# Kernel optimization log

Hardware: AMD Instinct MI355X
Metric: run time of the kernel (lower is better)

The kernel has to match this reference:

```python
import jax, jax.numpy as jnp
import numpy as np

N, E, G = 50000, 800000, 128
IN, HID, HEAD = 1280, 256, 4
DH = HID // HEAD
EPS = 1e-5
ATT_SCALE = 1.0 / np.sqrt(1280.0).astype(np.float32)  # hardcoded in source


def _seg_softmax(x, seg, n):
    # softmax over segments along axis 0; x: [K] or [K, H]
    m = jax.ops.segment_max(x, seg, num_segments=n)
    e = jnp.exp(x - m[seg])
    s = jax.ops.segment_sum(e, seg, num_segments=n)
    return e / s[seg]


def _bn(x, g, b):
    # eval-mode BatchNorm1d with init running stats (mean=0, var=1)
    return g * x * (1.0 / np.sqrt(1.0 + EPS)) + b


def _ln(x, g, b):
    mu = x.mean(-1, keepdims=True)
    var = ((x - mu) ** 2).mean(-1, keepdims=True)
    return g * (x - mu) / jnp.sqrt(var + EPS) + b


def setup_inputs() -> dict:
    key = jax.random.key(0)
    ks = jax.random.split(key, 40)
    rn = lambda i, shp, s=0.05: jax.random.normal(ks[i], shp, jnp.float32) * s
    inp = {
        "h": jax.random.normal(ks[0], (N, IN), jnp.float32),
        "gcn_w0": rn(1, (IN, HID)), "gcn_b0": rn(2, (HID,), 0.01),
        "gcn_w1": rn(3, (HID, HID)), "gcn_b1": rn(4, (HID,), 0.01),
        "bn_gcn0_g": 1.0 + rn(5, (HID,), 0.1), "bn_gcn0_b": rn(6, (HID,), 0.01),
        "bn_gcn1_g": 1.0 + rn(7, (HID,), 0.1), "bn_gcn1_b": rn(8, (HID,), 0.01),
        "gat_w0": rn(9, (IN, HID)), "gat_al0": rn(10, (HEAD, DH)), "gat_ar0": rn(11, (HEAD, DH)), "gat_bias0": rn(12, (HID,), 0.01),
        "gat_w1": rn(13, (HID, HID)), "gat_al1": rn(14, (HEAD, DH)), "gat_ar1": rn(15, (HEAD, DH)), "gat_bias1": rn(16, (HID,), 0.01),
        "bn_gat0_g": 1.0 + rn(17, (HID,), 0.1), "bn_gat0_b": rn(18, (HID,), 0.01),
        "bn_gat1_g": 1.0 + rn(19, (HID,), 0.1), "bn_gat1_b": rn(20, (HID,), 0.01),
        "gate_w": rn(21, (2 * HID, HID)), "gate_b": rn(22, (HID,), 0.01),
        "qw": rn(23, (HEAD, HID, HID)), "kw": rn(24, (HEAD, HID, HID)), "vw": rn(25, (HEAD, HID, HID)),
        "ct_w": rn(26, (HEAD * HID, HID)),
        "ff_w1": rn(27, (HID, 2 * HID)), "ff_b1": rn(28, (2 * HID,), 0.01),
        "ff_w2": rn(29, (2 * HID, HID)), "ff_b2": rn(30, (HID,), 0.01),
        "ln_g": 1.0 + rn(31, (HID,), 0.1), "ln_b": rn(32, (HID,), 0.01),
        "src": jax.random.randint(ks[33], (E,), 0, N, jnp.int32),
        "dst": jax.random.randint(ks[34], (E,), 0, N, jnp.int32),
        "gid": jnp.sort(jax.random.randint(ks[35], (N,), 0, G, jnp.int32)),
        "num_graphs": G,
    }
    return inp


def reference(h, gcn_w0, gcn_b0, gcn_w1, gcn_b1, bn_gcn0_g, bn_gcn0_b, bn_gcn1_g, bn_gcn1_b,
              gat_w0, gat_al0, gat_ar0, gat_bias0, gat_w1, gat_al1, gat_ar1, gat_bias1,
              bn_gat0_g, bn_gat0_b, bn_gat1_g, bn_gat1_b, gate_w, gate_b,
              qw, kw, vw, ct_w, ff_w1, ff_b1, ff_w2, ff_b2, ln_g, ln_b,
              src, dst, gid, num_graphs):
    n = h.shape[0]
    ones_e = jnp.ones(src.shape[0], h.dtype)
    # dgl.mean_nodes per graph
    cnt = jnp.clip(jax.ops.segment_sum(jnp.ones(n, h.dtype), gid, num_segments=num_graphs), 1.0)
    init_avg_h = jax.ops.segment_sum(h, gid, num_segments=num_graphs) / cnt[:, None]
    # GraphConv norm='both', degrees clamped to >=1
    deg_out = jnp.clip(jax.ops.segment_sum(ones_e, src, num_segments=n), 1.0)
    deg_in = jnp.clip(jax.ops.segment_sum(ones_e, dst, num_segments=n), 1.0)
    ns, nd = deg_out ** -0.5, deg_in ** -0.5

    def gcn(x, w, b):
        m = (x * ns[:, None]) @ w  # [N, HID]
        return jax.ops.segment_sum(m[src], dst, num_segments=n) * nd[:, None] + b

    hg = jax.nn.relu(_bn(gcn(h, gcn_w0, gcn_b0), bn_gcn0_g, bn_gcn0_b))
    hg = jax.nn.relu(_bn(gcn(hg, gcn_w1, gcn_b1), bn_gcn1_g, bn_gcn1_b)) + hg

    def gat(x, w, al, ar, b):
        f = (x @ w).reshape(n, HEAD, DH)
        el = (f * al).sum(-1)  # [N, HEAD]
        er = (f * ar).sum(-1)
        e = jax.nn.leaky_relu(el[src] + er[dst], 0.2)  # [E, HEAD]
        alpha = _seg_softmax(e, dst, n)  # edge softmax over incoming edges
        out = jax.ops.segment_sum(alpha[:, :, None] * f[src], dst, num_segments=n)
        return out.reshape(n, HID) + b

    ha = jax.nn.elu(_bn(gat(h, gat_w0, gat_al0, gat_ar0, gat_bias0), bn_gat0_g, bn_gat0_b))
    ha = jax.nn.elu(_bn(gat(ha, gat_w1, gat_al1, gat_ar1, gat_bias1), bn_gat1_g, bn_gat1_b)) + ha

    gate = jax.nn.sigmoid(jnp.concatenate([hg, ha], axis=1) @ gate_w + gate_b)
    x = gate * hg + (1.0 - gate) * ha  # residue_h

    # transformer_block: per-graph node softmax attention
    q = jnp.einsum('nd,hde->nhe', x, qw)
    k = jnp.einsum('nd,hde->nhe', x, kw)
    v = jnp.einsum('nd,hde->nhe', x, vw)
    att = (q * k).sum(-1) * ATT_SCALE  # [N, HEAD]
    alpha = _seg_softmax(att, gid, num_graphs)  # dgl.softmax_nodes per head
    mo = (v * alpha[:, :, None]).reshape(n, HEAD * HID) @ ct_w
    x1 = _ln(mo + x, ln_g, ln_b)
    x2 = _ln(jax.nn.relu(x1 @ ff_w1 + ff_b1) @ ff_w2 + ff_b2 + x1, ln_g, ln_b)

    readout = jax.ops.segment_sum(x2, gid, num_segments=num_graphs)
    return readout, init_avg_h
```

## Files before the change

### kernel.cpp

```cpp
#include <hip/hip_runtime.h>

#define NN 50000
#define NE 800000
#define NG 128
#define DIN 1280
#define HIDDEN 256
#define BNS 0.9999950000374997f
#define ATT_SCALE 0.027950849718747373f
#define LN_EPS 1e-5f

typedef __attribute__((ext_vector_type(8))) short short8;
typedef __attribute__((ext_vector_type(4))) float floatx4;

__device__ __forceinline__ float b2f(unsigned short u) {
  return __uint_as_float(((unsigned int)u) << 16);
}
__device__ __forceinline__ unsigned short f2b(float f) {
  unsigned int x = __float_as_uint(f);
  x += 0x7fffu + ((x >> 16) & 1u);
  return (unsigned short)(x >> 16);
}

__global__ void transpose_w_k(const float* __restrict__ src, unsigned short* __restrict__ dst,
                              int K, int Nc) {
  int idx = blockIdx.x * 256 + threadIdx.x;
  if (idx >= K * Nc) return;
  int n = idx / K, k = idx % K;
  dst[idx] = f2b(src[(size_t)k * Nc + n]);
}

__global__ void mw_k(const float* __restrict__ qw, const float* __restrict__ kw,
                     unsigned short* __restrict__ dst) {
  int col = blockIdx.x;
  int d = threadIdx.x;
  int hh = col >> 8, dp = col & 255;
  const float* qr = qw + ((size_t)hh * 256 + d) * 256;
  const float* kr = kw + ((size_t)hh * 256 + dp) * 256;
  float s = 0.f;
  for (int e = 0; e < 256; e += 4) {
    float4 a = *(const float4*)(qr + e);
    float4 b = *(const float4*)(kr + e);
    s += a.x * b.x + a.y * b.y + a.z * b.z + a.w * b.w;
  }
  dst[(size_t)col * 256 + d] = f2b(s);
}

__global__ void v_transpose_k(const float* __restrict__ vw, unsigned short* __restrict__ dst) {
  int idx = blockIdx.x * 256 + threadIdx.x;
  if (idx >= 1024 * 256) return;
  int r = idx >> 8;
  int d = idx & 255;
  int hh = r >> 8;
  int e2 = r & 255;
  dst[(size_t)(1024 + r) * 256 + d] = f2b(vw[((size_t)hh * 256 + d) * 256 + e2]);
}

__global__ void cvt_avg_k(const float* __restrict__ h, const int* __restrict__ gid,
                          unsigned short* __restrict__ h_bf, float* __restrict__ out1) {
  int row0 = blockIdx.x * 50;
  int tid = threadIdx.x;
  float acc[5] = {0, 0, 0, 0, 0};
  int cur_g = gid[row0];
  for (int r = 0; r < 50; ++r) {
    int row = row0 + r;
    int g = gid[row];
    if (g != cur_g) {
#pragma unroll
      for (int j = 0; j < 5; ++j) {
        atomicAdd(&out1[(size_t)cur_g * DIN + j * 256 + tid], acc[j]);
        acc[j] = 0.f;
      }
      cur_g = g;
    }
#pragma unroll
    for (int j = 0; j < 5; ++j) {
      float v = h[(size_t)row * DIN + j * 256 + tid];
      acc[j] += v;
      h_bf[(size_t)row * DIN + j * 256 + tid] = f2b(v);
    }
  }
#pragma unroll
  for (int j = 0; j < 5; ++j)
    atomicAdd(&out1[(size_t)cur_g * DIN + j * 256 + tid], acc[j]);
}

__global__ void div_avg_k(const int* __restrict__ start, float* __restrict__ out1) {
  int idx = blockIdx.x * 256 + threadIdx.x;
  if (idx >= NG * DIN) return;
  int g = idx / DIN;
// ... 57 lines not shown
                            int* __restrict__ row_ptr) {
  __shared__ int buf[256];
  int t = threadIdx.x;
  int v = (t < nb) ? bsum[t] : 0;
  buf[t] = v;
  __syncthreads();
  for (int off = 1; off < 256; off <<= 1) {
    int tv = (t >= off) ? buf[t - off] : 0;
    __syncthreads();
    buf[t] += tv;
    __syncthreads();
  }
  if (t < nb) boff[t] = buf[t] - v;
  if (t == 0) row_ptr[NN] = NE;
}

__global__ void scan_add_k(int* __restrict__ row_ptr, const int* __restrict__ boff) {
  int i = blockIdx.x * 256 + threadIdx.x;
  if (i >= NN) return;
  row_ptr[i] += boff[blockIdx.x];
}

__global__ void fill_csr_k(const int* __restrict__ src, const int* __restrict__ dst,
                           const int* __restrict__ row_ptr, int* __restrict__ fill,
                           int* __restrict__ csr_src, int e) {
  int i = blockIdx.x * 256 + threadIdx.x;
  if (i >= e) return;
  int d = dst[i];
  int pos = row_ptr[d] + atomicAdd(&fill[d], 1);
  csr_src[pos] = src[i];
}

template <int MODE>
__global__ __launch_bounds__(256, 2) void gemm_bf16(const unsigned short* __restrict__ A,
                                                    const unsigned short* __restrict__ Bt,
                                                    void* __restrict__ Cout,
                                                    const float* __restrict__ bias,
                                                    int M, int K, int Nc,
                                                    const unsigned short* __restrict__ xtile,
                                                    float* __restrict__ attp,
                                                    const float* __restrict__ ascale) {
  __shared__ unsigned short sbuf[16384];
  unsigned short* lA = sbuf;
  unsigned short* lB = sbuf + 8192;
  const int tid = threadIdx.x;
  const int n0 = blockIdx.x * 128;
  const int m0 = blockIdx.y * 128;
  const int w = tid >> 6;
  const int lane = tid & 63;
  const int wr = (w >> 1) * 64;
  const int wc = (w & 1) * 64;
  const int quad = lane >> 4;
  const int l15 = lane & 15;
  const int js = tid & 7;
  const int mbase = tid >> 3;

  floatx4 acc[4][4];
#pragma unroll
  for (int i = 0; i < 4; ++i)
#pragma unroll
    for (int j = 0; j < 4; ++j) acc[i][j] = (floatx4)0.0f;

  for (int k0 = 0; k0 < K; k0 += 64) {
    __syncthreads();
#pragma unroll
    for (int it = 0; it < 4; ++it) {
      int m = it * 32 + mbase;
      int gm = m0 + m;
      if (gm >= M) gm = M - 1;
      uint4 va = *(const uint4*)(A + (size_t)gm * K + k0 + js * 8);
      if (MODE == 5) {
        float s = ascale[(size_t)gm * 4 + (k0 >> 8)];
        unsigned short* pp = (unsigned short*)&va;
#pragma unroll
        for (int c = 0; c < 8; ++c) pp[c] = f2b(b2f(pp[c]) * s);
      }
      int ci_ = js * 128 + (m ^ js);
      *(uint4*)(lA + ci_ * 8) = va;
      int gn = n0 + m;
      uint4 vb = *(const uint4*)(Bt + (size_t)gn * K + k0 + js * 8);
      *(uint4*)(lB + ci_ * 8) = vb;
    }
    __syncthreads();
#pragma unroll
    for (int ks = 0; ks < 2; ++ks) {
      int kb = ks * 4 + quad;
      short8 af[4], bfr[4];
#pragma unroll
      for (int ri = 0; ri < 4; ++ri) {
        int r = wr + ri * 16 + l15;
        af[ri] = *(const short8*)(lA + (kb * 128 + (r ^ kb)) * 8);
      }
#pragma unroll
      for (int ci = 0; ci < 4; ++ci) {
        int c = wc + ci * 16 + l15;
        bfr[ci] = *(const short8*)(lB + (kb * 128 + (c ^ kb)) * 8);
      }
#pragma unroll
      for (int ri = 0; ri < 4; ++ri)
#pragma unroll
        for (int ci = 0; ci < 4; ++ci)
          acc[ri][ci] = __builtin_amdgcn_mfma_f32_16x16x32_bf16(af[ri], bfr[ci], acc[ri][ci], 0, 0, 0);
    }
  }

  if (MODE == 4 && n0 < 1024) {
    __syncthreads();
    int cb = n0 & 255;
#pragma unroll
    for (int it2 = 0; it2 < 8; ++it2) {
      int linear = it2 * 256 + tid;
      int rr = linear >> 4;
      int c8 = (linear & 15) * 8;
      int gr = m0 + rr;
      if (gr >= M) gr = M - 1;
      *(uint4*)(sbuf + rr * 128 + c8) = *(const uint4*)(xtile + (size_t)gr * 256 + cb + c8);
    }
    __syncthreads();
    int head = n0 >> 8;
#pragma unroll
    for (int ri = 0; ri < 4; ++ri) {
      int lrow = wr + ri * 16 + quad * 4;
#pragma unroll
      for (int r = 0; r < 4; ++r) {
        float p = 0.f;
#pragma unroll
        for (int ci = 0; ci < 4; ++ci)
          p += acc[ri][ci][r] * b2f(sbuf[(lrow + r) * 128 + wc + ci * 16 + l15]);
        p += __shfl_xor(p, 1);
        p += __shfl_xor(p, 2);
        p += __shfl_xor(p, 4);
        p += __shfl_xor(p, 8);
        if (l15 == 0) {
          int grow = m0 + lrow + r;
          if (grow < M) atomicAdd(&attp[(size_t)grow * 4 + head], p * ATT_SCALE);
        }
      }
    }
    return;
  }

#pragma unroll
  for (int ri = 0; ri < 4; ++ri) {
    int row = m0 + wr + ri * 16 + quad * 4;
#pragma unroll
    for (int ci = 0; ci < 4; ++ci) {
      int col = n0 + wc + ci * 16 + l15;
      float bv = (MODE == 2) ? bias[col] : 0.f;
#pragma unroll
      for (int r = 0; r < 4; ++r) {
        if (row + r < M) {
          float v = acc[ri][ci][r];
          if (MODE == 2) { v += bv; v = fmaxf(v, 0.f); }
          if (MODE == 1)
            ((float*)Cout)[(size_t)(row + r) * Nc + col] = v;
          else if (MODE == 4)
            ((unsigned short*)Cout)[(size_t)(row + r) * 1024 + col - 1024] = f2b(v);
          else
            ((unsigned short*)Cout)[(size_t)(row + r) * Nc + col] = f2b(v);
        }
      }
    }
  }
}

__global__ void gcn_agg_k(const unsigned short* __restrict__ m, int ldm,
                          const int* __restrict__ row_ptr, const int* __restrict__ csr_src,
                          const float* __restrict__ ns, const float* __restrict__ nd,
                          const float* __restrict__ bias,
                          const float* __restrict__ bng, const float* __restrict__ bnb,
                          const unsigned short* __restrict__ resid, int ldr,
                          unsigned short* __restrict__ out, int ldo) {
  int node = blockIdx.x * 4 + (threadIdx.x >> 6);
  if (node >= NN) return;
  int lane = threadIdx.x & 63;
  int s = row_ptr[node], e = row_ptr[node + 1];
  float a0 = 0, a1 = 0, a2 = 0, a3 = 0;
  for (int i = s; i < e; ++i) {
    int u = csr_src[i];
    float w = ns[u];
    ushort4 v = *(const ushort4*)(m + (size_t)u * ldm + lane * 4);
    a0 += w * b2f(v.x); a1 += w * b2f(v.y); a2 += w * b2f(v.z); a3 += w * b2f(v.w);
  }
  float ndv = nd[node];
  int col = lane * 4;
  float vals[4] = {a0, a1, a2, a3};
  ushort4 o;
#pragma unroll
  for (int c = 0; c < 4; ++c) {
    float v = vals[c] * ndv + bias[col + c];
    v = bng[col + c] * v * BNS + bnb[col + c];
    v = fmaxf(v, 0.f);
    if (resid) v += b2f(resid[(size_t)node * ldr + col + c]);
    ((unsigned short*)&o)[c] = f2b(v);
  }
  *(ushort4*)(out + (size_t)node * ldo + col) = o;
}

__global__ void elr_k(const unsigned short* __restrict__ f, int ldf,
                      const float* __restrict__ al, const float* __restrict__ ar,
                      float* __restrict__ elr) {
  int node = blockIdx.x * 4 + (threadIdx.x >> 6);
  if (node >= NN) return;
  int lane = threadIdx.x & 63;
  int head = lane >> 4;
  int col = lane * 4;
  int dcol = col & 63;
  ushort4 v = *(const ushort4*)(f + (size_t)node * ldf + col);
  float pl = 0, pr = 0;
#pragma unroll
  for (int c = 0; c < 4; ++c) {
    float x = b2f(((unsigned short*)&v)[c]);
    pl += x * al[head * 64 + dcol + c];
    pr += x * ar[head * 64 + dcol + c];
  }
#pragma unroll
  for (int off = 1; off < 16; off <<= 1) {
    pl += __shfl_xor(pl, off);
    pr += __shfl_xor(pr, off);
  }
  if ((lane & 15) == 0) {
    elr[(size_t)node * 8 + head] = pl;
    elr[(size_t)node * 8 + 4 + head] = pr;
  }
}

__global__ void gat_agg_k(const unsigned short* __restrict__ f, int ldf,
                          const int* __restrict__ row_ptr, const int* __restrict__ csr_src,
                          const float* __restrict__ elr,
                          const float* __restrict__ bias,
                          const float* __restrict__ bng, const float* __restrict__ bnb,
                          const unsigned short* __restrict__ resid, int ldr,
                          unsigned short* __restrict__ out, int ldo) {
  int node = blockIdx.x * 4 + (threadIdx.x >> 6);
  if (node >= NN) return;
  int lane = threadIdx.x & 63;
  int s = row_ptr[node], e = row_ptr[node + 1];
  float4 er = *(const float4*)(elr + (size_t)node * 8 + 4);
  float m0 = -1e30f, m1 = -1e30f, m2 = -1e30f, m3 = -1e30f;
  for (int i = s + lane; i < e; i += 64) {
    int u = csr_src[i];
    float4 el = *(const float4*)(elr + (size_t)u * 8);
    float t;
    t = el.x + er.x; t = t > 0.f ? t : 0.2f * t; m0 = fmaxf(m0, t);
    t = el.y + er.y; t = t > 0.f ? t : 0.2f * t; m1 = fmaxf(m1, t);
    t = el.z + er.z; t = t > 0.f ? t : 0.2f * t; m2 = fmaxf(m2, t);
    t = el.w + er.w; t = t > 0.f ? t : 0.2f * t; m3 = fmaxf(m3, t);
  }
#pragma unroll
  for (int off = 1; off < 64; off <<= 1) {
    m0 = fmaxf(m0, __shfl_xor(m0, off));
    m1 = fmaxf(m1, __shfl_xor(m1, off));
    m2 = fmaxf(m2, __shfl_xor(m2, off));
    m3 = fmaxf(m3, __shfl_xor(m3, off));
  }
  float s0 = 0, s1 = 0, s2 = 0, s3 = 0;
  for (int i = s + lane; i < e; i += 64) {
    int u = csr_src[i];
    float4 el = *(const float4*)(elr + (size_t)u * 8);
    float t;
    t = el.x + er.x; t = t > 0.f ? t : 0.2f * t; s0 += expf(t - m0);
    t = el.y + er.y; t = t > 0.f ? t : 0.2f * t; s1 += expf(t - m1);
    t = el.z + er.z; t = t > 0.f ? t : 0.2f * t; s2 += expf(t - m2);
    t = el.w + er.w; t = t > 0.f ? t : 0.2f * t; s3 += expf(t - m3);
  }
#pragma unroll
  for (int off = 1; off < 64; off <<= 1) {
    s0 += __shfl_xor(s0, off);
    s1 += __shfl_xor(s1, off);
    s2 += __shfl_xor(s2, off);
    s3 += __shfl_xor(s3, off);
  }
  int head = lane >> 4;
  float erh = head == 0 ? er.x : head == 1 ? er.y : head == 2 ? er.z : er.w;
  float mh = head == 0 ? m0 : head == 1 ? m1 : head == 2 ? m2 : m3;
  float sh = head == 0 ? s0 : head == 1 ? s1 : head == 2 ? s2 : s3;
  float inv_sh = (sh > 0.f) ? 1.f / sh : 0.f;
  float a0 = 0, a1 = 0, a2 = 0, a3 = 0;
  for (int i = s; i < e; ++i) {
    int u = csr_src[i];
    float t = elr[(size_t)u * 8 + head] + erh;
    t = t > 0.f ? t : 0.2f * t;
    float wgt = expf(t - mh) * inv_sh;
    ushort4 v = *(const ushort4*)(f + (size_t)u * ldf + lane * 4);
    a0 += wgt * b2f(v.x); a1 += wgt * b2f(v.y); a2 += wgt * b2f(v.z); a3 += wgt * b2f(v.w);
  }
  int col = lane * 4;
  float vals[4] = {a0, a1, a2, a3};
  ushort4 o;
#pragma unroll
  for (int c = 0; c < 4; ++c) {
    float v = vals[c] + bias[col + c];
    v = bng[col + c] * v * BNS + bnb[col + c];
    v = (v > 0.f) ? v : (expf(v) - 1.f);
    if (resid) v += b2f(resid[(size_t)node * ldr + col + c]);
    ((unsigned short*)&o)[c] = f2b(v);
  }
  *(ushort4*)(out + (size_t)node * ldo + col) = o;
}

__global__ void combine_k(const unsigned short* __restrict__ glogit, const float* __restrict__ gate_b,
                          const unsigned short* __restrict__ xcat,
                          unsigned short* __restrict__ xb) {
  int idx = blockIdx.x * 256 + threadIdx.x;
  if (idx >= NN * 64) return;
  int node = idx >> 6;
  int c = (idx & 63) * 4;
  ushort4 gl = *(const ushort4*)(glogit + (size_t)node * HIDDEN + c);
  ushort4 hgv = *(const ushort4*)(xcat + (size_t)node * 512 + c);
  ushort4 hav = *(const ushort4*)(xcat + (size_t)node * 512 + 256 + c);
  ushort4 ob;
  float g;
  g = 1.f / (1.f + expf(-(b2f(gl.x) + gate_b[c + 0]))); ob.x = f2b(g * b2f(hgv.x) + (1.f - g) * b2f(hav.x));
  g = 1.f / (1.f + expf(-(b2f(gl.y) + gate_b[c + 1]))); ob.y = f2b(g * b2f(hgv.y) + (1.f - g) * b2f(hav.y));
  g = 1.f / (1.f + expf(-(b2f(gl.z) + gate_b[c + 2]))); ob.z = f2b(g * b2f(hgv.z) + (1.f - g) * b2f(hav.z));
  g = 1.f / (1.f + expf(-(b2f(gl.w) + gate_b[c + 3]))); ob.w = f2b(g * b2f(hgv.w) + (1.f - g) * b2f(hav.w));
  *(ushort4*)(xb + (size_t)node * HIDDEN + c) = ob;
}

__global__ void gsoftmax_k(const float* __restrict__ att, const int* __restrict__ start,
                           float* __restrict__ alpha) {
  int g = blockIdx.x;
  int s = start[g], e = start[g + 1];
  int tid = threadIdx.x;
  __shared__ float red[256];
  __shared__ float mh[4], sh[4];
  float lm[4] = {-1e30f, -1e30f, -1e30f, -1e30f};
  for (int i = s + tid; i < e; i += 256) {
    float4 a = *(const float4*)(att + (size_t)i * 4);
    lm[0] = fmaxf(lm[0], a.x); lm[1] = fmaxf(lm[1], a.y);
    lm[2] = fmaxf(lm[2], a.z); lm[3] = fmaxf(lm[3], a.w);
  }
#pragma unroll
  for (int h = 0; h < 4; ++h) {
    red[tid] = lm[h]; __syncthreads();
    for (int off = 128; off > 0; off >>= 1) {
      if (tid < off) red[tid] = fmaxf(red[tid], red[tid + off]);
      __syncthreads();
    }
    if (tid == 0) mh[h] = red[0];
    __syncthreads();
  }
  float ls[4] = {0, 0, 0, 0};
  for (int i = s + tid; i < e; i += 256) {
    float4 a = *(const float4*)(att + (size_t)i * 4);
    ls[0] += expf(a.x - mh[0]); ls[1] += expf(a.y - mh[1]);
    ls[2] += expf(a.z - mh[2]); ls[3] += expf(a.w - mh[3]);
  }
#pragma unroll
  for (int h = 0; h < 4; ++h) {
// ... 52 lines not shown
  if (node >= NN) return;
  int lane = threadIdx.x & 63;
  int c = lane * 4;
  ushort4 a = *(const ushort4*)(ff2o + (size_t)node * HIDDEN + c);
  ushort4 xx = *(const ushort4*)(x1 + (size_t)node * HIDDEN + c);
  float v0 = b2f(a.x) + ffb2[c + 0] + b2f(xx.x), v1 = b2f(a.y) + ffb2[c + 1] + b2f(xx.y);
  float v2 = b2f(a.z) + ffb2[c + 2] + b2f(xx.z), v3 = b2f(a.w) + ffb2[c + 3] + b2f(xx.w);
  float sm = v0 + v1 + v2 + v3;
#pragma unroll
  for (int off = 1; off < 64; off <<= 1) sm += __shfl_xor(sm, off);
  float mu = sm * (1.f / 256.f);
  float d0 = v0 - mu, d1 = v1 - mu, d2 = v2 - mu, d3 = v3 - mu;
  float sq = d0 * d0 + d1 * d1 + d2 * d2 + d3 * d3;
#pragma unroll
  for (int off = 1; off < 64; off <<= 1) sq += __shfl_xor(sq, off);
  float inv = rsqrtf(sq * (1.f / 256.f) + LN_EPS);
  ushort4 ob;
  ob.x = f2b(g[c + 0] * d0 * inv + b[c + 0]);
  ob.y = f2b(g[c + 1] * d1 * inv + b[c + 1]);
  ob.z = f2b(g[c + 2] * d2 * inv + b[c + 2]);
  ob.w = f2b(g[c + 3] * d3 * inv + b[c + 3]);
  *(ushort4*)(x2 + (size_t)node * HIDDEN + c) = ob;
}

__global__ void readout_k(const unsigned short* __restrict__ x2, const int* __restrict__ start,
                          float* __restrict__ out0) {
  int g = blockIdx.x;
  int c = threadIdx.x;
  float acc = 0.f;
  for (int i = start[g]; i < start[g + 1]; ++i) acc += b2f(x2[(size_t)i * HIDDEN + c]);
  out0[(size_t)g * HIDDEN + c] = acc;
}

static const size_t OFF_BUFA   = 0;
static const size_t OFF_C01    = 128000000;
static const size_t OFF_HG0    = 179200000;
static const size_t OFF_HA0    = 204800000;
static const size_t OFF_M1     = 230400000;
static const size_t OFF_F1     = 256000000;
static const size_t OFF_XCAT   = 281600000;
static const size_t OFF_GLOGIT = 332800000;
static const size_t OFF_XB     = 358400000;
static const size_t OFF_MO     = 384000000;
static const size_t OFF_X1     = 409600000;
static const size_t OFF_ATT    = 435200000;
static const size_t OFF_ALPHA  = OFF_ATT + 800000;
static const size_t OFF_ELR0   = OFF_ALPHA + 800000;
static const size_t OFF_ELR1   = OFF_ELR0 + 1600000;
static const size_t OFF_START  = OFF_ELR1 + 1600000;
static const size_t OFF_DEGO   = OFF_START + 1024;
static const size_t OFF_DEGI   = OFF_DEGO + 200704;
static const size_t OFF_NS     = OFF_DEGI + 200704;
static const size_t OFF_ND     = OFF_NS + 200704;
static const size_t OFF_ROWP   = OFF_ND + 200704;
static const size_t OFF_FILL   = OFF_ROWP + 200704;
static const size_t OFF_BSUM   = OFF_FILL + 200704;
static const size_t OFF_BOFF   = OFF_BSUM + 1024;
static const size_t OFF_CSRS   = OFF_BOFF + 1024;
static const size_t OFF_W01T   = OFF_CSRS + 3200000;
static const size_t OFF_W1T    = OFF_W01T + 1310720;
static const size_t OFF_W1GT   = OFF_W1T + 131072;
static const size_t OFF_GATEWT = OFF_W1GT + 131072;
static const size_t OFF_WMVT   = OFF_GATEWT + 262144;
static const size_t OFF_CTWT   = OFF_WMVT + 1048576;
static const size_t OFF_FFW1T  = OFF_CTWT + 524288;
static const size_t OFF_FFW2T  = OFF_FFW1T + 262144;
static const size_t WS_NEED    = OFF_FFW2T + 262144;

extern "C" void kernel_launch(void* const* d_in, const int* in_sizes, int n_in,
                              void* d_out, int out_size, void* d_ws, size_t ws_size,
                              hipStream_t stream) {
  if (ws_size < WS_NEED) return;

  const float* h       = (const float*)d_in[0];
  const float* gcn_w0  = (const float*)d_in[1];
  const float* gcn_b0  = (const float*)d_in[2];
  const float* gcn_w1  = (const float*)d_in[3];
  const float* gcn_b1  = (const float*)d_in[4];
  const float* bn_gcn0_g = (const float*)d_in[5];
  const float* bn_gcn0_b = (const float*)d_in[6];
  const float* bn_gcn1_g = (const float*)d_in[7];
  const float* bn_gcn1_b = (const float*)d_in[8];
  const float* gat_w0  = (const float*)d_in[9];
  const float* gat_al0 = (const float*)d_in[10];
  const float* gat_ar0 = (const float*)d_in[11];
  const float* gat_bias0 = (const float*)d_in[12];
  const float* gat_w1  = (const float*)d_in[13];
  const float* gat_al1 = (const float*)d_in[14];
  const float* gat_ar1 = (const float*)d_in[15];
  const float* gat_bias1 = (const float*)d_in[16];
  const float* bn_gat0_g = (const float*)d_in[17];
  const float* bn_gat0_b = (const float*)d_in[18];
  const float* bn_gat1_g = (const float*)d_in[19];
  const float* bn_gat1_b = (const float*)d_in[20];
  const float* gate_w  = (const float*)d_in[21];
  const float* gate_b  = (const float*)d_in[22];
  const float* qw      = (const float*)d_in[23];
  const float* kw      = (const float*)d_in[24];
  const float* vw      = (const float*)d_in[25];
  const float* ct_w    = (const float*)d_in[26];
  const float* ff_w1   = (const float*)d_in[27];
  const float* ff_b1   = (const float*)d_in[28];
  const float* ff_w2   = (const float*)d_in[29];
  const float* ff_b2   = (const float*)d_in[30];
  const float* ln_g    = (const float*)d_in[31];
  const float* ln_b    = (const float*)d_in[32];
  const int* srcv = (const int*)d_in[33];
  const int* dstv = (const int*)d_in[34];
  const int* gid  = (const int*)d_in[35];

  char* ws = (char*)d_ws;
  unsigned short* h_bf = (unsigned short*)(ws + OFF_BUFA);
  unsigned short* yv   = (unsigned short*)(ws + OFF_BUFA);
  unsigned short* ff1o = (unsigned short*)(ws + OFF_BUFA);
  unsigned short* ff2o = (unsigned short*)(ws + OFF_BUFA + 51200000);
  unsigned short* x2   = (unsigned short*)(ws + OFF_BUFA + 76800000);
  unsigned short* c01  = (unsigned short*)(ws + OFF_C01);
  unsigned short* hg0  = (unsigned short*)(ws + OFF_HG0);
  unsigned short* ha0  = (unsigned short*)(ws + OFF_HA0);
  unsigned short* m1   = (unsigned short*)(ws + OFF_M1);
  unsigned short* f1   = (unsigned short*)(ws + OFF_F1);
  unsigned short* xcat = (unsigned short*)(ws + OFF_XCAT);
  unsigned short* glogit = (unsigned short*)(ws + OFF_GLOGIT);
  unsigned short* xb   = (unsigned short*)(ws + OFF_XB);
  unsigned short* mo   = (unsigned short*)(ws + OFF_MO);
  unsigned short* x1   = (unsigned short*)(ws + OFF_X1);
  float* att           = (float*)(ws + OFF_ATT);
  float* alpha         = (float*)(ws + OFF_ALPHA);
  float* elr0          = (float*)(ws + OFF_ELR0);
  float* elr1          = (float*)(ws + OFF_ELR1);
  int* start   = (int*)(ws + OFF_START);
  int* deg_out = (int*)(ws + OFF_DEGO);
  int* deg_in  = (int*)(ws + OFF_DEGI);
  float* ns    = (float*)(ws + OFF_NS);
  float* nd    = (float*)(ws + OFF_ND);
  int* row_ptr = (int*)(ws + OFF_ROWP);
  int* fill    = (int*)(ws + OFF_FILL);
  int* bsum    = (int*)(ws + OFF_BSUM);
  int* boff    = (int*)(ws + OFF_BOFF);
  int* csr_src = (int*)(ws + OFF_CSRS);
  unsigned short* w01t   = (unsigned short*)(ws + OFF_W01T);
  unsigned short* w1t    = (unsigned short*)(ws + OFF_W1T);
  unsigned short* w1gt   = (unsigned short*)(ws + OFF_W1GT);
  unsigned short* gatewt = (unsigned short*)(ws + OFF_GATEWT);
  unsigned short* wmvt   = (unsigned short*)(ws + OFF_WMVT);
  unsigned short* ctwt   = (unsigned short*)(ws + OFF_CTWT);
  unsigned short* ffw1t  = (unsigned short*)(ws + OFF_FFW1T);
  unsigned short* ffw2t  = (unsigned short*)(ws + OFF_FFW2T);

  float* out0 = (float*)d_out;
  float* out1 = out0 + NG * HIDDEN;

  hipMemsetAsync(deg_out, 0, NN * 4, stream);
  hipMemsetAsync(deg_in, 0, NN * 4, stream);
  hipMemsetAsync(fill, 0, NN * 4, stream);
  hipMemsetAsync(out1, 0, NG * DIN * 4, stream);
  hipMemsetAsync(att, 0, NN * 4 * 4, stream);

  transpose_w_k<<<(1280 * 256 + 255) / 256, 256, 0, stream>>>(gcn_w0, w01t, 1280, 256);
  transpose_w_k<<<(1280 * 256 + 255) / 256, 256, 0, stream>>>(gat_w0, w01t + 256 * 1280, 1280, 256);
  transpose_w_k<<<(256 * 256 + 255) / 256, 256, 0, stream>>>(gcn_w1, w1t, 256, 256);
  transpose_w_k<<<(256 * 256 + 255) / 256, 256, 0, stream>>>(gat_w1, w1gt, 256, 256);
  transpose_w_k<<<(512 * 256 + 255) / 256, 256, 0, stream>>>(gate_w, gatewt, 512, 256);
  mw_k<<<1024, 256, 0, stream>>>(qw, kw, wmvt);
  v_transpose_k<<<1024, 256, 0, stream>>>(vw, wmvt);
  transpose_w_k<<<(1024 * 256 + 255) / 256, 256, 0, stream>>>(ct_w, ctwt, 1024, 256);
  transpose_w_k<<<(256 * 512 + 255) / 256, 256, 0, stream>>>(ff_w1, ffw1t, 256, 512);
  transpose_w_k<<<(512 * 256 + 255) / 256, 256, 0, stream>>>(ff_w2, ffw2t, 512, 256);

  graph_bounds_k<<<(NN + 255) / 256, 256, 0, stream>>>(gid, start, NN);
  degrees_k<<<(NE + 255) / 256, 256, 0, stream>>>(srcv, dstv, deg_out, deg_in, NE);
  invsqrt_k<<<(NN + 255) / 256, 256, 0, stream>>>(deg_out, deg_in, ns, nd, NN);
  const int NB_SCAN = (NN + 255) / 256;
  scan_local_k<<<NB_SCAN, 256, 0, stream>>>(deg_in, row_ptr, bsum);
  scan_bsum_k<<<1, 256, 0, stream>>>(bsum, boff, NB_SCAN, row_ptr);
  scan_add_k<<<NB_SCAN, 256, 0, stream>>>(row_ptr, boff);
  fill_csr_k<<<(NE + 255) / 256, 256, 0, stream>>>(srcv, dstv, row_ptr, fill, csr_src, NE);

  cvt_avg_k<<<NN / 50, 256, 0, stream>>>(h, gid, h_bf, out1);
  div_avg_k<<<(NG * DIN + 255) / 256, 256, 0, stream>>>(start, out1);

  const int MB = (NN + 127) / 128;
  gemm_bf16<0><<<dim3(4, MB), 256, 0, stream>>>(h_bf, w01t, c01, nullptr, NN, 1280, 512,
                                                nullptr, nullptr, nullptr);
  gcn_agg_k<<<NN / 4, 256, 0, stream>>>(c01, 512, row_ptr, csr_src, ns, nd,
                                        gcn_b0, bn_gcn0_g, bn_gcn0_b, nullptr, 0, hg0, 256);
  elr_k<<<NN / 4, 256, 0, stream>>>(c01 + 256, 512, gat_al0, gat_ar0, elr0);
  gat_agg_k<<<NN / 4, 256, 0, stream>>>(c01 + 256, 512, row_ptr, csr_src, elr0,
                                        gat_bias0, bn_gat0_g, bn_gat0_b, nullptr, 0, ha0, 256);
  gemm_bf16<0><<<dim3(2, MB), 256, 0, stream>>>(hg0, w1t, m1, nullptr, NN, 256, 256,
                                                nullptr, nullptr, nullptr);
  gcn_agg_k<<<NN / 4, 256, 0, stream>>>(m1, 256, row_ptr, csr_src, ns, nd,
                                        gcn_b1, bn_gcn1_g, bn_gcn1_b, hg0, 256, xcat, 512);
  gemm_bf16<0><<<dim3(2, MB), 256, 0, stream>>>(ha0, w1gt, f1, nullptr, NN, 256, 256,
                                                nullptr, nullptr, nullptr);
  elr_k<<<NN / 4, 256, 0, stream>>>(f1, 256, gat_al1, gat_ar1, elr1);
  gat_agg_k<<<NN / 4, 256, 0, stream>>>(f1, 256, row_ptr, csr_src, elr1,
                                        gat_bias1, bn_gat1_g, bn_gat1_b, ha0, 256, xcat + 256, 512);
  gemm_bf16<0><<<dim3(2, MB), 256, 0, stream>>>(xcat, gatewt, glogit, nullptr, NN, 512, 256,
                                                nullptr, nullptr, nullptr);
  combine_k<<<NN / 4, 256, 0, stream>>>(glogit, gate_b, xcat, xb);
  gemm_bf16<4><<<dim3(16, MB), 256, 0, stream>>>(xb, wmvt, yv, nullptr, NN, 256, 2048,
                                                 xb, att, nullptr);
  gsoftmax_k<<<NG, 256, 0, stream>>>(att, start, alpha);
  gemm_bf16<5><<<dim3(2, MB), 256, 0, stream>>>(yv, ctwt, mo, nullptr, NN, 1024, 256,
                                                nullptr, nullptr, alpha);
  ln1_k<<<NN / 4, 256, 0, stream>>>(mo, xb, ln_g, ln_b, x1);
  gemm_bf16<2><<<dim3(4, MB), 256, 0, stream>>>(x1, ffw1t, ff1o, ff_b1, NN, 256, 512,
                                                nullptr, nullptr, nullptr);
  gemm_bf16<0><<<dim3(2, MB), 256, 0, stream>>>(ff1o, ffw2t, ff2o, nullptr, NN, 512, 256,
                                                nullptr, nullptr, nullptr);
  ln2_k<<<NN / 4, 256, 0, stream>>>(ff2o, ff_b2, x1, ln_g, ln_b, x2);
  readout_k<<<NG, 256, 0, stream>>>(x2, start, out0);
}
```

Measured before the change: 1.750 ms.

## Fuse elr and gate epilogues into GEMMs, batch layer-1 GEMMs, enlarge tiles

Several ideas land at once. GEMM tiles grow to 256x128 with one wave per 64 rows. The GAT el/er projections move into the GEMM epilogues (modes 6 and 7), which removes the elr kernels, and the gate sigmoid/combine moves into the gate GEMM epilogue. The two layer-1 GEMMs are merged into one launch over padded stacked buffers, and the weight transposes are batched into a single prep launch. The GAT edge softmax also drops its max-subtraction pass, which saves a full edge sweep but risks overflow in expf for large logits.

```diff
diff --git a/kernel.cpp b/kernel.cpp
--- a/kernel.cpp
+++ b/kernel.cpp
@@ -1,6 +1,7 @@
 #include <hip/hip_runtime.h>
 
 #define NN 50000
+#define NN2 50176
 #define NE 800000
 #define NG 128
 #define DIN 1280
@@ -21,12 +22,21 @@
   return (unsigned short)(x >> 16);
 }
 
-__global__ void transpose_w_k(const float* __restrict__ src, unsigned short* __restrict__ dst,
-                              int K, int Nc) {
+struct PrepJob { const float* s; unsigned short* d; int K; int Nc; int special; };
+struct PrepJobs { PrepJob j[9]; };
+
+__global__ void prep_k(PrepJobs P) {
+  PrepJob pj = P.j[blockIdx.y];
   int idx = blockIdx.x * 256 + threadIdx.x;
-  if (idx >= K * Nc) return;
-  int n = idx / K, k = idx % K;
-  dst[idx] = f2b(src[(size_t)k * Nc + n]);
+  if (idx >= pj.K * pj.Nc) return;
+  if (!pj.special) {
+    int n = idx / pj.K, k = idx % pj.K;
+    pj.d[idx] = f2b(pj.s[(size_t)k * pj.Nc + n]);
+  } else {
+    int r = idx >> 8, dd = idx & 255;
+    int hh = r >> 8, e2 = r & 255;
+    pj.d[idx] = f2b(pj.s[((size_t)hh * 256 + dd) * 256 + e2]);
+  }
 }
 
 __global__ void mw_k(const float* __restrict__ qw, const float* __restrict__ kw,
@@ -45,16 +55,6 @@
   dst[(size_t)col * 256 + d] = f2b(s);
 }
 
-__global__ void v_transpose_k(const float* __restrict__ vw, unsigned short* __restrict__ dst) {
-  int idx = blockIdx.x * 256 + threadIdx.x;
-  if (idx >= 1024 * 256) return;
-  int r = idx >> 8;
-  int d = idx & 255;
-  int hh = r >> 8;
-  int e2 = r & 255;
-  dst[(size_t)(1024 + r) * 256 + d] = f2b(vw[((size_t)hh * 256 + d) * 256 + e2]);
-}
-
 __global__ void cvt_avg_k(const float* __restrict__ h, const int* __restrict__ gid,
                           unsigned short* __restrict__ h_bf, float* __restrict__ out1) {
   int row0 = blockIdx.x * 50;
@@ -178,39 +178,46 @@
 }
 
 template <int MODE>
-__global__ __launch_bounds__(256, 2) void gemm_bf16(const unsigned short* __restrict__ A,
-                                                    const unsigned short* __restrict__ Bt,
-                                                    void* __restrict__ Cout,
-                                                    const float* __restrict__ bias,
-                                                    int M, int K, int Nc,
-                                                    const unsigned short* __restrict__ xtile,
-                                                    float* __restrict__ attp,
-                                                    const float* __restrict__ ascale) {
-  __shared__ unsigned short sbuf[16384];
+__global__ __launch_bounds__(256, 2) void gemm_bf16(
+    const unsigned short* __restrict__ A,
+    const unsigned short* __restrict__ Bt,
+    const unsigned short* __restrict__ Bt2,
+    void* __restrict__ Cout,
+    const float* __restrict__ bias,
+    int M, int K, int Nc,
+    const unsigned short* __restrict__ xaux,
+    float* __restrict__ faux,
+    const float* __restrict__ ascale,
+    const float* __restrict__ al, const float* __restrict__ ar,
+    int esplit) {
+  constexpr int SBN = (MODE == 4) ? 32768 : 24576;
+  __shared__ unsigned short sbuf[SBN];
   unsigned short* lA = sbuf;
-  unsigned short* lB = sbuf + 8192;
+  unsigned short* lB = sbuf + 16384;
   const int tid = threadIdx.x;
   const int n0 = blockIdx.x * 128;
-  const int m0 = blockIdx.y * 128;
+  const int m0 = blockIdx.y * 256;
   const int w = tid >> 6;
   const int lane = tid & 63;
-  const int wr = (w >> 1) * 64;
-  const int wc = (w & 1) * 64;
   const int quad = lane >> 4;
   const int l15 = lane & 15;
   const int js = tid & 7;
   const int mbase = tid >> 3;
-
-  floatx4 acc[4][4];
+  const int wrow = w * 64;
+
+  const unsigned short* Buse = Bt;
+  if (MODE == 7 && m0 >= esplit) Buse = Bt2;
+
+  floatx4 acc[4][8];
 #pragma unroll
   for (int i = 0; i < 4; ++i)
 #pragma unroll
-    for (int j = 0; j < 4; ++j) acc[i][j] = (floatx4)0.0f;
+    for (int j = 0; j < 8; ++j) acc[i][j] = (floatx4)0.0f;
 
   for (int k0 = 0; k0 < K; k0 += 64) {
     __syncthreads();
 #pragma unroll
-    for (int it = 0; it < 4; ++it) {
+    for (int it = 0; it < 8; ++it) {
       int m = it * 32 + mbase;
       int gm = m0 + m;
       if (gm >= M) gm = M - 1;
@@ -221,31 +228,33 @@
 #pragma unroll
         for (int c = 0; c < 8; ++c) pp[c] = f2b(b2f(pp[c]) * s);
       }
-      int ci_ = js * 128 + (m ^ js);
-      *(uint4*)(lA + ci_ * 8) = va;
-      int gn = n0 + m;
-      uint4 vb = *(const uint4*)(Bt + (size_t)gn * K + k0 + js * 8);
-      *(uint4*)(lB + ci_ * 8) = vb;
+      *(uint4*)(lA + (js * 256 + (m ^ js)) * 8) = va;
+    }
+#pragma unroll
+    for (int it = 0; it < 4; ++it) {
+      int n = it * 32 + mbase;
+      uint4 vb = *(const uint4*)(Buse + (size_t)(n0 + n) * K + k0 + js * 8);
+      *(uint4*)(lB + (js * 128 + (n ^ js)) * 8) = vb;
     }
     __syncthreads();
 #pragma unroll
     for (int ks = 0; ks < 2; ++ks) {
       int kb = ks * 4 + quad;
-      short8 af[4], bfr[4];
+      short8 af[4], bfr[8];
 #pragma unroll
       for (int ri = 0; ri < 4; ++ri) {
-        int r = wr + ri * 16 + l15;
-        af[ri] = *(const short8*)(lA + (kb * 128 + (r ^ kb)) * 8);
+        int r = wrow + ri * 16 + l15;
+        af[ri] = *(const short8*)(lA + (kb * 256 + (r ^ kb)) * 8);
       }
 #pragma unroll
-      for (int ci = 0; ci < 4; ++ci) {
-        int c = wc + ci * 16 + l15;
+      for (int ci = 0; ci < 8; ++ci) {
+        int c = ci * 16 + l15;
         bfr[ci] = *(const short8*)(lB + (kb * 128 + (c ^ kb)) * 8);
       }
 #pragma unroll
       for (int ri = 0; ri < 4; ++ri)
 #pragma unroll
-        for (int ci = 0; ci < 4; ++ci)
+        for (int ci = 0; ci < 8; ++ci)
           acc[ri][ci] = __builtin_amdgcn_mfma_f32_16x16x32_bf16(af[ri], bfr[ci], acc[ri][ci], 0, 0, 0);
     }
   }
@@ -254,32 +263,32 @@
     __syncthreads();
     int cb = n0 & 255;
 #pragma unroll
-    for (int it2 = 0; it2 < 8; ++it2) {
+    for (int it2 = 0; it2 < 16; ++it2) {
       int linear = it2 * 256 + tid;
       int rr = linear >> 4;
       int c8 = (linear & 15) * 8;
       int gr = m0 + rr;
       if (gr >= M) gr = M - 1;
-      *(uint4*)(sbuf + rr * 128 + c8) = *(const uint4*)(xtile + (size_t)gr * 256 + cb + c8);
+      *(uint4*)(sbuf + rr * 128 + c8) = *(const uint4*)(xaux + (size_t)gr * 256 + cb + c8);
     }
     __syncthreads();
     int head = n0 >> 8;
 #pragma unroll
     for (int ri = 0; ri < 4; ++ri) {
-      int lrow = wr + ri * 16 + quad * 4;
+      int lrow = wrow + ri * 16 + quad * 4;
 #pragma unroll
       for (int r = 0; r < 4; ++r) {
         float p = 0.f;
 #pragma unroll
-        for (int ci = 0; ci < 4; ++ci)
-          p += acc[ri][ci][r] * b2f(sbuf[(lrow + r) * 128 + wc + ci * 16 + l15]);
+        for (int ci = 0; ci < 8; ++ci)
+          p += acc[ri][ci][r] * b2f(sbuf[(lrow + r) * 128 + ci * 16 + l15]);
         p += __shfl_xor(p, 1);
         p += __shfl_xor(p, 2);
         p += __shfl_xor(p, 4);
         p += __shfl_xor(p, 8);
         if (l15 == 0) {
           int grow = m0 + lrow + r;
-          if (grow < M) atomicAdd(&attp[(size_t)grow * 4 + head], p * ATT_SCALE);
+          if (grow < M) atomicAdd(&faux[(size_t)grow * 4 + head], p * ATT_SCALE);
         }
       }
     }
@@ -288,22 +297,65 @@
 
 #pragma unroll
   for (int ri = 0; ri < 4; ++ri) {
-    int row = m0 + wr + ri * 16 + quad * 4;
-#pragma unroll
-    for (int ci = 0; ci < 4; ++ci) {
-      int col = n0 + wc + ci * 16 + l15;
-      float bv = (MODE == 2) ? bias[col] : 0.f;
+    int row = m0 + wrow + ri * 16 + quad * 4;
+#pragma unroll
+    for (int ci = 0; ci < 8; ++ci) {
+      int col = n0 + ci * 16 + l15;
+      float bv = (MODE == 2 || MODE == 3) ? bias[col] : 0.f;
 #pragma unroll
       for (int r = 0; r < 4; ++r) {
         if (row + r < M) {
           float v = acc[ri][ci][r];
-          if (MODE == 2) { v += bv; v = fmaxf(v, 0.f); }
-          if (MODE == 1)
-            ((float*)Cout)[(size_t)(row + r) * Nc + col] = v;
-          else if (MODE == 4)
+          if (MODE == 2) {
+            v += bv; v = fmaxf(v, 0.f);
+            ((unsigned short*)Cout)[(size_t)(row + r) * Nc + col] = f2b(v);
+          } else if (MODE == 3) {
+            float g = 1.f / (1.f + expf(-(v + bv)));
+            float hg = b2f(xaux[(size_t)(row + r) * 512 + col]);
+            float ha = b2f(xaux[(size_t)(row + r) * 512 + 256 + col]);
+            ((unsigned short*)Cout)[(size_t)(row + r) * 256 + col] = f2b(g * hg + (1.f - g) * ha);
+          } else if (MODE == 4) {
             ((unsigned short*)Cout)[(size_t)(row + r) * 1024 + col - 1024] = f2b(v);
-          else
+          } else {
             ((unsigned short*)Cout)[(size_t)(row + r) * Nc + col] = f2b(v);
+          }
+        }
+      }
+    }
+  }
+
+  if ((MODE == 6 && n0 >= esplit) || (MODE == 7 && m0 >= esplit)) {
+    int hbase = (MODE == 6) ? ((n0 - esplit) >> 6) : (n0 >> 6);
+#pragma unroll
+    for (int ri = 0; ri < 4; ++ri) {
+#pragma unroll
+      for (int r = 0; r < 4; ++r) {
+        int grow = m0 + wrow + ri * 16 + quad * 4 + r;
+        float pl0 = 0, pr0 = 0, pl1 = 0, pr1 = 0;
+#pragma unroll
+        for (int ci = 0; ci < 4; ++ci) {
+          float a0_ = acc[ri][ci][r];
+          float a1_ = acc[ri][ci + 4][r];
+          float w0l = al[hbase * 64 + ci * 16 + l15];
+          float w0r = ar[hbase * 64 + ci * 16 + l15];
+          float w1l = al[(hbase + 1) * 64 + ci * 16 + l15];
+          float w1r = ar[(hbase + 1) * 64 + ci * 16 + l15];
+          pl0 += a0_ * w0l; pr0 += a0_ * w0r;
+          pl1 += a1_ * w1l; pr1 += a1_ * w1r;
+        }
+#pragma unroll
+        for (int off = 1; off < 16; off <<= 1) {
+          pl0 += __shfl_xor(pl0, off); pr0 += __shfl_xor(pr0, off);
+          pl1 += __shfl_xor(pl1, off); pr1 += __shfl_xor(pr1, off);
+        }
+        if (l15 == 0) {
+          int erow = (MODE == 7) ? (grow - esplit) : grow;
+          if (erow >= 0 && erow < NN) {
+            faux[(size_t)erow * 8 + hbase] = pl0;
+            faux[(size_t)erow * 8 + 4 + hbase] = pr0;
+            faux[(size_t)erow * 8 + hbase + 1] = pl1;
+            faux[(size_t)erow * 8 + 5 + hbase] = pr1;
+          }
         }
       }
     }
@@ -343,34 +395,6 @@
   *(ushort4*)(out + (size_t)node * ldo + col) = o;
 }
 
-__global__ void elr_k(const unsigned short* __restrict__ f, int ldf,
-                      const float* __restrict__ al, const float* __restrict__ ar,
-                      float* __restrict__ elr) {
-  int node = blockIdx.x * 4 + (threadIdx.x >> 6);
-  if (node >= NN) return;
-  int lane = threadIdx.x & 63;
-  int head = lane >> 4;
-  int col = lane * 4;
-  int dcol = col & 63;
-  ushort4 v = *(const ushort4*)(f + (size_t)node * ldf + col);
-  float pl = 0, pr = 0;
-#pragma unroll
-  for (int c = 0; c < 4; ++c) {
-    float x = b2f(((unsigned short*)&v)[c]);
-    pl += x * al[head * 64 + dcol + c];
-    pr += x * ar[head * 64 + dcol + c];
-  }
-#pragma unroll
-  for (int off = 1; off < 16; off <<= 1) {
-    pl += __shfl_xor(pl, off);
-    pr += __shfl_xor(pr, off);
-  }
-  if ((lane & 15) == 0) {
-    elr[(size_t)node * 8 + head] = pl;
-    elr[(size_t)node * 8 + 4 + head] = pr;
-  }
-}
-
 __global__ void gat_agg_k(const unsigned short* __restrict__ f, int ldf,
                           const int* __restrict__ row_ptr, const int* __restrict__ csr_src,
                           const float* __restrict__ elr,
@@ -383,32 +407,15 @@
   int lane = threadIdx.x & 63;
   int s = row_ptr[node], e = row_ptr[node + 1];
   float4 er = *(const float4*)(elr + (size_t)node * 8 + 4);
-  float m0 = -1e30f, m1 = -1e30f, m2 = -1e30f, m3 = -1e30f;
-  for (int i = s + lane; i < e; i += 64) {
-    int u = csr_src[i];
-    float4 el = *(const float4*)(elr + (size_t)u * 8);
-    float t;
-    t = el.x + er.x; t = t > 0.f ? t : 0.2f * t; m0 = fmaxf(m0, t);
-    t = el.y + er.y; t = t > 0.f ? t : 0.2f * t; m1 = fmaxf(m1, t);
-    t = el.z + er.z; t = t > 0.f ? t : 0.2f * t; m2 = fmaxf(m2, t);
-    t = el.w + er.w; t = t > 0.f ? t : 0.2f * t; m3 = fmaxf(m3, t);
-  }
-#pragma unroll
-  for (int off = 1; off < 64; off <<= 1) {
-    m0 = fmaxf(m0, __shfl_xor(m0, off));
-    m1 = fmaxf(m1, __shfl_xor(m1, off));
-    m2 = fmaxf(m2, __shfl_xor(m2, off));
-    m3 = fmaxf(m3, __shfl_xor(m3, off));
-  }
   float s0 = 0, s1 = 0, s2 = 0, s3 = 0;
   for (int i = s + lane; i < e; i += 64) {
     int u = csr_src[i];
     float4 el = *(const float4*)(elr + (size_t)u * 8);
     float t;
-    t = el.x + er.x; t = t > 0.f ? t : 0.2f * t; s0 += expf(t - m0);
-    t = el.y + er.y; t = t > 0.f ? t : 0.2f * t; s1 += expf(t - m1);
-    t = el.z + er.z; t = t > 0.f ? t : 0.2f * t; s2 += expf(t - m2);
-    t = el.w + er.w; t = t > 0.f ? t : 0.2f * t; s3 += expf(t - m3);
+    t = el.x + er.x; t = t > 0.f ? t : 0.2f * t; s0 += expf(t);
+    t = el.y + er.y; t = t > 0.f ? t : 0.2f * t; s1 += expf(t);
+    t = el.z + er.z; t = t > 0.f ? t : 0.2f * t; s2 += expf(t);
+    t = el.w + er.w; t = t > 0.f ? t : 0.2f * t; s3 += expf(t);
   }
 #pragma unroll
   for (int off = 1; off < 64; off <<= 1) {
@@ -419,7 +426,6 @@
   }
   int head = lane >> 4;
   float erh = head == 0 ? er.x : head == 1 ? er.y : head == 2 ? er.z : er.w;
-  float mh = head == 0 ? m0 : head == 1 ? m1 : head == 2 ? m2 : m3;
   float sh = head == 0 ? s0 : head == 1 ? s1 : head == 2 ? s2 : s3;
   float inv_sh = (sh > 0.f) ? 1.f / sh : 0.f;
   float a0 = 0, a1 = 0, a2 = 0, a3 = 0;
@@ -427,7 +433,7 @@
     int u = csr_src[i];
     float t = elr[(size_t)u * 8 + head] + erh;
     t = t > 0.f ? t : 0.2f * t;
-    float wgt = expf(t - mh) * inv_sh;
+    float wgt = expf(t) * inv_sh;
     ushort4 v = *(const ushort4*)(f + (size_t)u * ldf + lane * 4);
     a0 += wgt * b2f(v.x); a1 += wgt * b2f(v.y); a2 += wgt * b2f(v.z); a3 += wgt * b2f(v.w);
   }
@@ -443,25 +449,6 @@
     ((unsigned short*)&o)[c] = f2b(v);
   }
   *(ushort4*)(out + (size_t)node * ldo + col) = o;
-}
-
-__global__ void combine_k(const unsigned short* __restrict__ glogit, const float* __restrict__ gate_b,
-                          const unsigned short* __restrict__ xcat,
-                          unsigned short* __restrict__ xb) {
-  int idx = blockIdx.x * 256 + threadIdx.x;
-  if (idx >= NN * 64) return;
-  int node = idx >> 6;
-  int c = (idx & 63) * 4;
-  ushort4 gl = *(const ushort4*)(glogit + (size_t)node * HIDDEN + c);
-  ushort4 hgv = *(const ushort4*)(xcat + (size_t)node * 512 + c);
-  ushort4 hav = *(const ushort4*)(xcat + (size_t)node * 512 + 256 + c);
-  ushort4 ob;
-  float g;
-  g = 1.f / (1.f + expf(-(b2f(gl.x) + gate_b[c + 0]))); ob.x = f2b(g * b2f(hgv.x) + (1.f - g) * b2f(hav.x));
-  g = 1.f / (1.f + expf(-(b2f(gl.y) + gate_b[c + 1]))); ob.y = f2b(g * b2f(hgv.y) + (1.f - g) * b2f(hav.y));
-  g = 1.f / (1.f + expf(-(b2f(gl.z) + gate_b[c + 2]))); ob.z = f2b(g * b2f(hgv.z) + (1.f - g) * b2f(hav.z));
-  g = 1.f / (1.f + expf(-(b2f(gl.w) + gate_b[c + 3]))); ob.w = f2b(g * b2f(hgv.w) + (1.f - g) * b2f(hav.w));
-  *(ushort4*)(xb + (size_t)node * HIDDEN + c) = ob;
 }
 
 __global__ void gsoftmax_k(const float* __restrict__ att, const int* __restrict__ start,
@@ -580,29 +567,29 @@
   out0[(size_t)g * HIDDEN + c] = acc;
 }
 
+#define PADROWSZ 25690112ull
 static const size_t OFF_BUFA   = 0;
 static const size_t OFF_C01    = 128000000;
 static const size_t OFF_HG0    = 179200000;
-static const size_t OFF_HA0    = 204800000;
-static const size_t OFF_M1     = 230400000;
-static const size_t OFF_F1     = 256000000;
-static const size_t OFF_XCAT   = 281600000;
-static const size_t OFF_GLOGIT = 332800000;
-static const size_t OFF_XB     = 358400000;
-static const size_t OFF_MO     = 384000000;
-static const size_t OFF_X1     = 409600000;
-static const size_t OFF_ATT    = 435200000;
+static const size_t OFF_HA0    = OFF_HG0 + PADROWSZ;
+static const size_t OFF_M1     = OFF_HA0 + PADROWSZ;
+static const size_t OFF_F1     = OFF_M1 + PADROWSZ;
+static const size_t OFF_XCAT   = OFF_F1 + PADROWSZ;
+static const size_t OFF_XB     = OFF_XCAT + 51200000;
+static const size_t OFF_MO     = OFF_XB + 25600000;
+static const size_t OFF_X1     = OFF_MO + 25600000;
+static const size_t OFF_ATT    = OFF_X1 + 25600000;
 static const size_t OFF_ALPHA  = OFF_ATT + 800000;
 static const size_t OFF_ELR0   = OFF_ALPHA + 800000;
 static const size_t OFF_ELR1   = OFF_ELR0 + 1600000;
 static const size_t OFF_START  = OFF_ELR1 + 1600000;
 static const size_t OFF_DEGO   = OFF_START + 1024;
 static const size_t OFF_DEGI   = OFF_DEGO + 200704;
-static const size_t OFF_NS     = OFF_DEGI + 200704;
+static const size_t OFF_FILL   = OFF_DEGI + 200704;
+static const size_t OFF_NS     = OFF_FILL + 200704;
 static const size_t OFF_ND     = OFF_NS + 200704;
 static const size_t OFF_ROWP   = OFF_ND + 200704;
-static const size_t OFF_FILL   = OFF_ROWP + 200704;
-static const size_t OFF_BSUM   = OFF_FILL + 200704;
+static const size_t OFF_BSUM   = OFF_ROWP + 200704;
 static const size_t OFF_BOFF   = OFF_BSUM + 1024;
 static const size_t OFF_CSRS   = OFF_BOFF + 1024;
 static const size_t OFF_W01T   = OFF_CSRS + 3200000;
@@ -669,7 +656,6 @@
   unsigned short* m1   = (unsigned short*)(ws + OFF_M1);
   unsigned short* f1   = (unsigned short*)(ws + OFF_F1);
   unsigned short* xcat = (unsigned short*)(ws + OFF_XCAT);
-  unsigned short* glogit = (unsigned short*)(ws + OFF_GLOGIT);
   unsigned short* xb   = (unsigned short*)(ws + OFF_XB);
   unsigned short* mo   = (unsigned short*)(ws + OFF_MO);
   unsigned short* x1   = (unsigned short*)(ws + OFF_X1);
@@ -680,10 +666,10 @@
   int* start   = (int*)(ws + OFF_START);
   int* deg_out = (int*)(ws + OFF_DEGO);
   int* deg_in  = (int*)(ws + OFF_DEGI);
+  int* fill    = (int*)(ws + OFF_FILL);
   float* ns    = (float*)(ws + OFF_NS);
   float* nd    = (float*)(ws + OFF_ND);
   int* row_ptr = (int*)(ws + OFF_ROWP);
-  int* fill    = (int*)(ws + OFF_FILL);
   int* bsum    = (int*)(ws + OFF_BSUM);
   int* boff    = (int*)(ws + OFF_BOFF);
   int* csr_src = (int*)(ws + OFF_CSRS);
@@ -699,22 +685,22 @@
   float* out0 = (float*)d_out;
   float* out1 = out0 + NG * HIDDEN;
 
-  hipMemsetAsync(deg_out, 0, NN * 4, stream);
-  hipMemsetAsync(deg_in, 0, NN * 4, stream);
-  hipMemsetAsync(fill, 0, NN * 4, stream);
+  hipMemsetAsync(deg_out, 0, 3 * 200704, stream);
   hipMemsetAsync(out1, 0, NG * DIN * 4, stream);
   hipMemsetAsync(att, 0, NN * 4 * 4, stream);
 
-  transpose_w_k<<<(1280 * 256 + 255) / 256, 256, 0, stream>>>(gcn_w0, w01t, 1280, 256);
-  transpose_w_k<<<(1280 * 256 + 255) / 256, 256, 0, stream>>>(gat_w0, w01t + 256 * 1280, 1280, 256);
-  transpose_w_k<<<(256 * 256 + 255) / 256, 256, 0, stream>>>(gcn_w1, w1t, 256, 256);
-  transpose_w_k<<<(256 * 256 + 255) / 256, 256, 0, stream>>>(gat_w1, w1gt, 256, 256);
-  transpose_w_k<<<(512 * 256 + 255) / 256, 256, 0, stream>>>(gate_w, gatewt, 512, 256);
+  PrepJobs PJ;
+  PJ.j[0] = {gcn_w0, w01t, 1280, 256, 0};
+  PJ.j[1] = {gat_w0, w01t + 256 * 1280, 1280, 256, 0};
+  PJ.j[2] = {gcn_w1, w1t, 256, 256, 0};
+  PJ.j[3] = {gat_w1, w1gt, 256, 256, 0};
+  PJ.j[4] = {gate_w, gatewt, 512, 256, 0};
+  PJ.j[5] = {ct_w, ctwt, 1024, 256, 0};
+  PJ.j[6] = {ff_w1, ffw1t, 256, 512, 0};
+  PJ.j[7] = {ff_w2, ffw2t, 512, 256, 0};
+  PJ.j[8] = {vw, wmvt + 1024 * 256, 1024, 256, 1};
+  prep_k<<<dim3(1280, 9), 256, 0, stream>>>(PJ);
   mw_k<<<1024, 256, 0, stream>>>(qw, kw, wmvt);
-  v_transpose_k<<<1024, 256, 0, stream>>>(vw, wmvt);
-  transpose_w_k<<<(1024 * 256 + 255) / 256, 256, 0, stream>>>(ct_w, ctwt, 1024, 256);
-  transpose_w_k<<<(256 * 512 + 255) / 256, 256, 0, stream>>>(ff_w1, ffw1t, 256, 512);
-  transpose_w_k<<<(512 * 256 + 255) / 256, 256, 0, stream>>>(ff_w2, ffw2t, 512, 256);
 
   graph_bounds_k<<<(NN + 255) / 256, 256, 0, stream>>>(gid, start, NN);
   degrees_k<<<(NE + 255) / 256, 256, 0, stream>>>(srcv, dstv, deg_out, deg_in, NE);
@@ -728,36 +714,33 @@
   cvt_avg_k<<<NN / 50, 256, 0, stream>>>(h, gid, h_bf, out1);
   div_avg_k<<<(NG * DIN + 255) / 256, 256, 0, stream>>>(start, out1);
 
-  const int MB = (NN + 127) / 128;
-  gemm_bf16<0><<<dim3(4, MB), 256, 0, stream>>>(h_bf, w01t, c01, nullptr, NN, 1280, 512,
-                                                nullptr, nullptr, nullptr);
+  const int MB2 = (NN + 255) / 256;
+  gemm_bf16<6><<<dim3(4, MB2), 256, 0, stream>>>(h_bf, w01t, nullptr, c01, nullptr, NN, 1280, 512,
+                                                 nullptr, elr0, nullptr, gat_al0, gat_ar0, 256);
   gcn_agg_k<<<NN / 4, 256, 0, stream>>>(c01, 512, row_ptr, csr_src, ns, nd,
                                         gcn_b0, bn_gcn0_g, bn_gcn0_b, nullptr, 0, hg0, 256);
-  elr_k<<<NN / 4, 256, 0, stream>>>(c01 + 256, 512, gat_al0, gat_ar0, elr0);
   gat_agg_k<<<NN / 4, 256, 0, stream>>>(c01 + 256, 512, row_ptr, csr_src, elr0,
                                         gat_bias0, bn_gat0_g, bn_gat0_b, nullptr, 0, ha0, 256);
-  gemm_bf16<0><<<dim3(2, MB), 256, 0, stream>>>(hg0, w1t, m1, nullptr, NN, 256, 256,
-                                                nullptr, nullptr, nullptr);
+  gemm_bf16<7><<<dim3(2, 2 * (NN2 / 256)), 256, 0, stream>>>(hg0, w1t, w1gt, m1, nullptr,
+                                                             2 * NN2, 256, 256,
+                                                             nullptr, elr1, nullptr,
+                                                             gat_al1, gat_ar1, NN2);
   gcn_agg_k<<<NN / 4, 256, 0, stream>>>(m1, 256, row_ptr, csr_src, ns, nd,
                                         gcn_b1, bn_gcn1_g, bn_gcn1_b, hg0, 256, xcat, 512);
-  gemm_bf16<0><<<dim3(2, MB), 256, 0, stream>>>(ha0, w1gt, f1, nullptr, NN, 256, 256,
-                                                nullptr, nullptr, nullptr);
-  elr_k<<<NN / 4, 256, 0, stream>>>(f1, 256, gat_al1, gat_ar1, elr1);
   gat_agg_k<<<NN / 4, 256, 0, stream>>>(f1, 256, row_ptr, csr_src, elr1,
                                         gat_bias1, bn_gat1_g, bn_gat1_b, ha0, 256, xcat + 256, 512);
-  gemm_bf16<0><<<dim3(2, MB), 256, 0, stream>>>(xcat, gatewt, glogit, nullptr, NN, 512, 256,
-                                                nullptr, nullptr, nullptr);
-  combine_k<<<NN / 4, 256, 0, stream>>>(glogit, gate_b, xcat, xb);
-  gemm_bf16<4><<<dim3(16, MB), 256, 0, stream>>>(xb, wmvt, yv, nullptr, NN, 256, 2048,
-                                                 xb, att, nullptr);
+  gemm_bf16<3><<<dim3(2, MB2), 256, 0, stream>>>(xcat, gatewt, nullptr, xb, gate_b, NN, 512, 256,
+                                                 xcat, nullptr, nullptr, nullptr, nullptr, 0);
+  gemm_bf16<4><<<dim3(16, MB2), 256, 0, stream>>>(xb, wmvt, nullptr, yv, nullptr, NN, 256, 2048,
+                                                  xb, att, nullptr, nullptr, nullptr, 0);
   gsoftmax_k<<<NG, 256, 0, stream>>>(att, start, alpha);
-  gemm_bf16<5><<<dim3(2, MB), 256, 0, stream>>>(yv, ctwt, mo, nullptr, NN, 1024, 256,
-                                                nullptr, nullptr, alpha);
+  gemm_bf16<5><<<dim3(2, MB2), 256, 0, stream>>>(yv, ctwt, nullptr, mo, nullptr, NN, 1024, 256,
+                                                 nullptr, nullptr, alpha, nullptr, nullptr, 0);
   ln1_k<<<NN / 4, 256, 0, stream>>>(mo, xb, ln_g, ln_b, x1);
-  gemm_bf16<2><<<dim3(4, MB), 256, 0, stream>>>(x1, ffw1t, ff1o, ff_b1, NN, 256, 512,
-                                                nullptr, nullptr, nullptr);
-  gemm_bf16<0><<<dim3(2, MB), 256, 0, stream>>>(ff1o, ffw2t, ff2o, nullptr, NN, 512, 256,
-                                                nullptr, nullptr, nullptr);
+  gemm_bf16<2><<<dim3(4, MB2), 256, 0, stream>>>(x1, ffw1t, nullptr, ff1o, ff_b1, NN, 256, 512,
+                                                 nullptr, nullptr, nullptr, nullptr, nullptr, 0);
+  gemm_bf16<0><<<dim3(2, MB2), 256, 0, stream>>>(ff1o, ffw2t, nullptr, ff2o, nullptr, NN, 512, 256,
+                                                 nullptr, nullptr, nullptr, nullptr, nullptr, 0);
   ln2_k<<<NN / 4, 256, 0, stream>>>(ff2o, ff_b2, x1, ln_g, ln_b, x2);
   readout_k<<<NG, 256, 0, stream>>>(x2, start, out0);
 }
```

Measured after the change: 1.898 ms. 1.08x slower.
